# Optimization experiments

Measured on AMD Instinct MI355X. Metric: run time of the kernel, lower is better.

The kernel has to match this reference:

```python
import jax, jax.numpy as jnp
import numpy as np

B, C, T = 8, 256, 4096
IC = C // 2  # inter_channels
BN_EPS = 1e-5


def setup_inputs() -> dict:
    key = jax.random.key(0)
    ks = jax.random.split(key, 12)
    s_in = 1.0 / np.sqrt(C)
    s_ic = 1.0 / np.sqrt(IC)
    return {
        "x": jax.random.normal(ks[0], (B, C, T), dtype=jnp.float32),
        "theta_w": jax.random.uniform(ks[1], (IC, C), jnp.float32, -s_in, s_in),
        "theta_b": jax.random.uniform(ks[2], (IC,), jnp.float32, -s_in, s_in),
        "phi_w": jax.random.uniform(ks[3], (IC, C), jnp.float32, -s_in, s_in),
        "phi_b": jax.random.uniform(ks[4], (IC,), jnp.float32, -s_in, s_in),
        "g_w": jax.random.uniform(ks[5], (IC, C), jnp.float32, -s_in, s_in),
        "g_b": jax.random.uniform(ks[6], (IC,), jnp.float32, -s_in, s_in),
        "w_w": jax.random.uniform(ks[7], (C, IC), jnp.float32, -s_ic, s_ic),
        "w_b": jax.random.uniform(ks[8], (C,), jnp.float32, -s_ic, s_ic),
        "bn_gamma": jax.random.normal(ks[9], (C,), dtype=jnp.float32),
        "bn_beta": jax.random.normal(ks[10], (C,), dtype=jnp.float32),
    }


def _conv1x1(w, b, inp):
    # Conv1d kernel_size=1 == per-position channel matmul
    return jnp.einsum('oc,bct->bot', w, inp) + b[None, :, None]


def _maxpool2(z):
    b, c, t = z.shape
    return z.reshape(b, c, t // 2, 2).max(axis=-1)


def reference(x, theta_w, theta_b, phi_w, phi_b, g_w, g_b, w_w, w_b, bn_gamma, bn_beta):
    theta_x = _conv1x1(theta_w, theta_b, x)              # (B, IC, T)
    phi_x = _maxpool2(_conv1x1(phi_w, phi_b, x))         # (B, IC, T/2)
    g_x = _maxpool2(_conv1x1(g_w, g_b, x))               # (B, IC, T/2)

    # f = theta^T @ phi ; softmax-free, divided by N = T/2
    f = jnp.einsum('bct,bcs->bts', theta_x, phi_x)       # (B, T, T/2)
    f_div_C = f / f.shape[-1]
    y = jnp.einsum('bts,bcs->bct', f_div_C, g_x)         # (B, IC, T)

    w_y = _conv1x1(w_w, w_b, y)                          # (B, C, T)
    # BatchNorm1d (training-mode batch statistics over batch+time)
    mean = w_y.mean(axis=(0, 2), keepdims=True)
    var = w_y.var(axis=(0, 2), keepdims=True)
    w_y = (w_y - mean) * jax.lax.rsqrt(var + BN_EPS)
    w_y = w_y * bn_gamma[None, :, None] + bn_beta[None, :, None]
    return w_y + x
```

## Files before the change

kernel.cpp:

```cpp
#include <hip/hip_runtime.h>
#include <hip/hip_bf16.h>

typedef __attribute__((ext_vector_type(8))) short short8;
typedef __attribute__((ext_vector_type(4))) short short4v;
typedef __attribute__((ext_vector_type(4))) float floatx4;
typedef unsigned int u32;

#define BB 8
#define CC 256
#define ICH 128
#define TT 4096
#define SS 2048
static constexpr float BN_EPS = 1e-5f;
static constexpr float INV_S  = 1.0f / 2048.0f;
static constexpr float INV_BT = 1.0f / 32768.0f;

typedef const __attribute__((address_space(1))) u32* gas_ptr;
typedef __attribute__((address_space(3))) u32* las_ptr;
__device__ __forceinline__ void gl_lds16(const void* g, void* l) {
    __builtin_amdgcn_global_load_lds((gas_ptr)g, (las_ptr)l, 16, 0, 0);
}


__global__ __launch_bounds__(256) void k0x_transpose(
    const float* __restrict__ x, __hip_bfloat16* __restrict__ xt,
    const float* __restrict__ phi_w, const float* __restrict__ g_w,
    __hip_bfloat16* __restrict__ Wf)
{
    const int id = blockIdx.x;
    if (id >= 2048) {
        int idx = (id - 2048) * 256 + threadIdx.x;
        const float* src = (idx < 8192) ? (phi_w + (size_t)idx * 4)
                                        : (g_w + (size_t)(idx - 8192) * 4);
        float4 v = *(const float4*)src;
        alignas(8) __hip_bfloat16 t[4];
        t[0] = __float2bfloat16(v.x); t[1] = __float2bfloat16(v.y);
        t[2] = __float2bfloat16(v.z); t[3] = __float2bfloat16(v.w);
        *(short4v*)(Wf + (size_t)idx * 4) = *(const short4v*)t;
        return;
    }

    __shared__ float Tl[64][65];
    const int b = id & 7, rest = id >> 3;
    const int cb = (rest & 3) * 64, tb = (rest >> 2) * 64;
    const int tid = threadIdx.x;
    #pragma unroll
    for (int it = 0; it < 4; ++it) {
        int idx = tid + 256 * it;
        int row = idx >> 4, c4 = idx & 15;
        float4 v = *(const float4*)(x + ((size_t)b * CC + cb + row) * TT + tb + c4 * 4);
        Tl[row][c4 * 4 + 0] = v.x; Tl[row][c4 * 4 + 1] = v.y;
        Tl[row][c4 * 4 + 2] = v.z; Tl[row][c4 * 4 + 3] = v.w;
    }
    __syncthreads();
    #pragma unroll
    for (int it = 0; it < 2; ++it) {
        int idx = tid + 256 * it;
        int trow = idx >> 3, ch = idx & 7;
        alignas(16) __hip_bfloat16 tmp[8];
        #pragma unroll
        for (int e = 0; e < 8; ++e) tmp[e] = __float2bfloat16(Tl[ch * 8 + e][trow]);
        *(short8*)(xt + ((size_t)b * TT + tb + trow) * CC + cb + ch * 8) = *(const short8*)tmp;
    }
}

__global__ __launch_bounds__(256) void k1_mfma(
    const __hip_bfloat16* __restrict__ Wf, const float* __restrict__ phi_b,
    const float* __restrict__ g_b, const __hip_bfloat16* __restrict__ xt,
    __hip_bfloat16* __restrict__ phi_g)
{
    __shared__ short lds[128 * 132];
    short* As = lds;
    short* Bs = lds + 128 * 64;

    const int id = blockIdx.x;
    const int b  = id & 7;
    const int m0 = ((id >> 3) & 1) * 128;
    const int tb = (id >> 4) * 128;
    const int s0 = (id >> 4) * 64;
    const int tid = threadIdx.x;
    const int w = tid >> 6, l = tid & 63;
    const int quad = l >> 4, lm = l & 15;
    const int wm = (w & 1) * 64, wn = (w >> 1) * 64;
    const int rs = l >> 3, cs = (l & 7) * 8;

    const __hip_bfloat16* Ap = Wf + (size_t)m0 * CC;
    const __hip_bfloat16* Bp = xt + ((size_t)b * TT + tb) * CC;

    floatx4 acc[4][4];
    #pragma unroll
    for (int i = 0; i < 4; ++i)
        #pragma unroll
        for (int j = 0; j < 4; ++j) acc[i][j] = (floatx4)0.f;

    for (int kc = 0; kc < 4; ++kc) {
        const int k0 = kc * 64;
        const int rbase = w * 32;
        #pragma unroll
        for (int t = 0; t < 4; ++t) {
            gl_lds16(Ap + (size_t)(rbase + t * 8 + rs) * CC + k0 + cs, &As[(rbase + t * 8) * 64]);
            gl_lds16(Bp + (size_t)(rbase + t * 8 + rs) * CC + k0 + cs, &Bs[(rbase + t * 8) * 64]);
        }
        __syncthreads();
        #pragma unroll
        for (int ks = 0; ks < 2; ++ks) {
            short8 a[4], bb[4];
            #pragma unroll
            for (int i = 0; i < 4; ++i)
                a[i] = *(const short8*)&As[(wm + i * 16 + lm) * 64 + ks * 32 + quad * 8];
            #pragma unroll
            for (int j = 0; j < 4; ++j)
                bb[j] = *(const short8*)&Bs[(wn + j * 16 + lm) * 64 + ks * 32 + quad * 8];
            #pragma unroll
            for (int i = 0; i < 4; ++i)
                #pragma unroll
                for (int j = 0; j < 4; ++j)
                    acc[i][j] = __builtin_amdgcn_mfma_f32_16x16x32_bf16(a[i], bb[j], acc[i][j], 0, 0, 0);
        }
        __syncthreads();
    }

    __hip_bfloat16* Out = (__hip_bfloat16*)lds;
    #pragma unroll
    for (int i = 0; i < 4; ++i)
        #pragma unroll
        for (int j = 0; j < 4; ++j)
            #pragma unroll
            for (int r = 0; r < 4; ++r)
                Out[(wm + i * 16 + quad * 4 + r) * 132 + wn + j * 16 + lm] =
                    __float2bfloat16(acc[i][j][r]);
    __syncthreads();
    #pragma unroll
    for (int it = 0; it < 4; ++it) {
        int idx = tid + 256 * it;
        int orow = idx >> 3, grp = idx & 7;
        int o = m0 + orow;
        float bias = (o < ICH) ? phi_b[o] : g_b[o - ICH];
        short8 v0 = *(const short8*)&Out[orow * 132 + grp * 16];
        short8 v1 = *(const short8*)&Out[orow * 132 + grp * 16 + 8];
        const __hip_bfloat16* p0 = (const __hip_bfloat16*)&v0;
        const __hip_bfloat16* p1 = (const __hip_bfloat16*)&v1;
        alignas(16) __hip_bfloat16 o8[8];
        #pragma unroll
        for (int e = 0; e < 4; ++e)
            o8[e] = __float2bfloat16(
                fmaxf(__bfloat162float(p0[2 * e]), __bfloat162float(p0[2 * e + 1])) + bias);
        #pragma unroll
        for (int e = 0; e < 4; ++e)
            o8[4 + e] = __float2bfloat16(
                fmaxf(__bfloat162float(p1[2 * e]), __bfloat162float(p1[2 * e + 1])) + bias);
        *(short8*)(phi_g + ((size_t)b * CC + o) * SS + s0 + grp * 8) = *(const short8*)o8;
    }
}

__global__ __launch_bounds__(256) void k2_mfma(
    const __hip_bfloat16* __restrict__ phi_g, float* __restrict__ Mpart)
{
    __shared__ short lds[2 * 128 * 64];
    short* As = lds;
    short* Bs = lds + 128 * 64;
    const int b = blockIdx.x, sc = blockIdx.y;
    const int tid = threadIdx.x;
    const int w = tid >> 6, l = tid & 63;
    const int quad = l >> 4, lm = l & 15;
    const int wm = (w & 1) * 64, wn = (w >> 1) * 64;
    const int rs = l >> 3, cs = (l & 7) * 8;

    const __hip_bfloat16* Ap = phi_g + (size_t)b * CC * SS + (size_t)ICH * SS + sc * 256;
    const __hip_bfloat16* Bp = phi_g + (size_t)b * CC * SS + sc * 256;

    floatx4 acc[4][4];
    #pragma unroll
    for (int i = 0; i < 4; ++i)
        #pragma unroll
        for (int j = 0; j < 4; ++j) acc[i][j] = (floatx4)0.f;

    for (int kc = 0; kc < 4; ++kc) {
        const int k0 = kc * 64;
        const int rbase = w * 32;
        #pragma unroll
        for (int t = 0; t < 4; ++t) {
            gl_lds16(Ap + (size_t)(rbase + t * 8 + rs) * SS + k0 + cs, &As[(rbase + t * 8) * 64]);
            gl_lds16(Bp + (size_t)(rbase + t * 8 + rs) * SS + k0 + cs, &Bs[(rbase + t * 8) * 64]);
        }
        __syncthreads();
        #pragma unroll
        for (int ks = 0; ks < 2; ++ks) {
            short8 a[4], bb[4];
            #pragma unroll
            for (int i = 0; i < 4; ++i)
                a[i] = *(const short8*)&As[(wm + i * 16 + lm) * 64 + ks * 32 + quad * 8];
            #pragma unroll
            for (int j = 0; j < 4; ++j)
                bb[j] = *(const short8*)&Bs[(wn + j * 16 + lm) * 64 + ks * 32 + quad * 8];
            #pragma unroll
            for (int i = 0; i < 4; ++i)
                #pragma unroll
                for (int j = 0; j < 4; ++j)
                    acc[i][j] = __builtin_amdgcn_mfma_f32_16x16x32_bf16(a[i], bb[j], acc[i][j], 0, 0, 0);
        }
        __syncthreads();
    }

    float* dst = Mpart + ((size_t)(b * 8 + sc)) * ICH * ICH;
    #pragma unroll
    for (int i = 0; i < 4; ++i)
        #pragma unroll
        for (int j = 0; j < 4; ++j)
            #pragma unroll
            for (int r = 0; r < 4; ++r)
                dst[(size_t)(wm + i * 16 + quad * 4 + r) * ICH + wn + j * 16 + lm] = acc[i][j][r];
}

__global__ __launch_bounds__(256) void kpq(
    const float* __restrict__ w_w, const float* __restrict__ Mpart,
    const float* __restrict__ theta_w, const float* __restrict__ theta_b,
    const float* __restrict__ w_b, __hip_bfloat16* __restrict__ P,
    float* __restrict__ q)
{
    __shared__ float Ms[128][128];
    __shared__ float Al[128][68];
    const int bid = blockIdx.x;
    const int b    = bid & 7;
    const int rest = bid >> 3;
    const int cob  = (rest >> 2) * 64;
    const int cib  = (rest & 3) * 64;
    const int tid = threadIdx.x;
    const int tx = tid & 15, ty = tid >> 4;

    {
        const float* src = Mpart + (size_t)b * 8 * ICH * ICH;
        #pragma unroll
        for (int e = 0; e < 16; ++e) {
            int f = e * 256 + tid;
            float4 s = *(const float4*)(src + (size_t)f * 4);
            #pragma unroll
            for (int sc = 1; sc < 8; ++sc) {
                float4 m = *(const float4*)(src + (size_t)sc * ICH * ICH + (size_t)f * 4);
                s.x += m.x; s.y += m.y; s.z += m.z; s.w += m.w;
            }
            *(float4*)&Ms[f >> 5][(f & 31) * 4] = s;
        }
    }
    #pragma unroll
    for (int it = 0; it < 8; ++it) {
        int idx = tid + 256 * it;
        int row = idx & 63, c4 = idx >> 6;
        float4 v = *(const float4*)(w_w + (size_t)(cob + row) * ICH + c4 * 4);
        Al[c4 * 4 + 0][row] = v.x; Al[c4 * 4 + 1][row] = v.y;
        Al[c4 * 4 + 2][row] = v.z; Al[c4 * 4 + 3][row] = v.w;
    }
    __syncthreads();

    float accK[4][8] = {};
    #pragma unroll 4
    for (int k = 0; k < 128; ++k) {
        float4 av = *(const float4*)&Al[k][ty * 4];
        float4 b0 = *(const float4*)&Ms[k][tx * 4];
        float4 b1 = *(const float4*)&Ms[k][64 + tx * 4];
        const float* avp = (const float*)&av;
        const float* b0p = (const float*)&b0;
        const float* b1p = (const float*)&b1;
        #pragma unroll
        for (int i = 0; i < 4; ++i) {
            #pragma unroll
            for (int j = 0; j < 4; ++j) {
                accK[i][j]     += avp[i] * b0p[j];
                accK[i][4 + j] += avp[i] * b1p[j];
            }
        }
    }
    __syncthreads();

    float (*KbL)[68] = Al;
    #pragma unroll
    for (int i = 0; i < 4; ++i)
        #pragma unroll
        for (int jj = 0; jj < 8; ++jj)
            KbL[(jj >> 2) * 64 + tx * 4 + (jj & 3)][ty * 4 + i] = accK[i][jj] * INV_S;
    __syncthreads();

    float acc[4][4] = {};
    #pragma unroll 8
    for (int k = 0; k < 128; ++k) {
        float4 av = *(const float4*)&KbL[k][ty * 4];
        float4 bv = *(const float4*)(theta_w + (size_t)k * CC + cib + tx * 4);
        const float* avp = (const float*)&av;
        const float* bvp = (const float*)&bv;
        #pragma unroll
        for (int i = 0; i < 4; ++i)
            #pragma unroll
            for (int j = 0; j < 4; ++j)
                acc[i][j] += avp[i] * bvp[j];
    }
    #pragma unroll
    for (int i = 0; i < 4; ++i) {
        alignas(8) __hip_bfloat16 o4[4];
        #pragma unroll
        for (int j = 0; j < 4; ++j) o4[j] = __float2bfloat16(acc[i][j]);
        *(short4v*)(P + ((size_t)b * CC + cob + ty * 4 + i) * CC + cib + tx * 4) =
            *(const short4v*)o4;
    }

    if ((rest & 3) == 0 && tid < 64) {
        float s = w_b[cob + tid];
        #pragma unroll 8
        for (int c = 0; c < ICH; ++c) s += KbL[c][tid] * theta_b[c];
        q[b * CC + cob + tid] = s;
    }
}

__global__ __launch_bounds__(256) void k4_mfma(
    const __hip_bfloat16* __restrict__ P, const __hip_bfloat16* __restrict__ xt,
    const float* __restrict__ q, __hip_bfloat16* __restrict__ wy,
    float* __restrict__ pbuf)
{
    __shared__ short lds[128 * 132];
    __shared__ float pst1[4 * 64], pst2[4 * 64];
    short* As = lds;
    short* Bs = lds + 128 * 64;

    const int id = blockIdx.x;
    const int b  = id & 7;
    const int m0 = ((id >> 3) & 1) * 128;
    const int tt = id >> 4;
    const int t0 = tt * 128;
    const int tid = threadIdx.x;
    const int w = tid >> 6, l = tid & 63;
    const int quad = l >> 4, lm = l & 15;
    const int wm = (w & 1) * 64, wn = (w >> 1) * 64;
    const int rs = l >> 3, cs = (l & 7) * 8;

    const __hip_bfloat16* Ap = P + ((size_t)b * CC + m0) * CC;
    const __hip_bfloat16* Bp = xt + ((size_t)b * TT + t0) * CC;

    floatx4 acc[4][4];
    #pragma unroll
    for (int i = 0; i < 4; ++i)
        #pragma unroll
        for (int j = 0; j < 4; ++j) acc[i][j] = (floatx4)0.f;

    for (int kc = 0; kc < 4; ++kc) {
        const int k0 = kc * 64;
        const int rbase = w * 32;
        #pragma unroll
        for (int t = 0; t < 4; ++t) {
            gl_lds16(Ap + (size_t)(rbase + t * 8 + rs) * CC + k0 + cs, &As[(rbase + t * 8) * 64]);
            gl_lds16(Bp + (size_t)(rbase + t * 8 + rs) * CC + k0 + cs, &Bs[(rbase + t * 8) * 64]);
        }
        __syncthreads();
        #pragma unroll
        for (int ks = 0; ks < 2; ++ks) {
            short8 a[4], bb[4];
            #pragma unroll
            for (int i = 0; i < 4; ++i)
                a[i] = *(const short8*)&As[(wm + i * 16 + lm) * 64 + ks * 32 + quad * 8];
            #pragma unroll
            for (int j = 0; j < 4; ++j)
                bb[j] = *(const short8*)&Bs[(wn + j * 16 + lm) * 64 + ks * 32 + quad * 8];
            #pragma unroll
            for (int i = 0; i < 4; ++i)
                #pragma unroll
                for (int j = 0; j < 4; ++j)
                    acc[i][j] = __builtin_amdgcn_mfma_f32_16x16x32_bf16(a[i], bb[j], acc[i][j], 0, 0, 0);
        }
        __syncthreads();
    }

    #pragma unroll
    for (int i = 0; i < 4; ++i) {
        #pragma unroll
        for (int r = 0; r < 4; ++r) {
            int m = wm + i * 16 + quad * 4 + r;
            float bias = q[b * CC + m0 + m];
            float s1 = 0.f, s2 = 0.f;
            #pragma unroll
            for (int j = 0; j < 4; ++j) {
                float v = acc[i][j][r] + bias;
                s1 += v; s2 += v * v;
            }
            #pragma unroll
            for (int off = 1; off < 16; off <<= 1) {
                s1 += __shfl_xor(s1, off);
                s2 += __shfl_xor(s2, off);
            }
            if (lm == 0) {
                pst1[w * 64 + i * 16 + quad * 4 + r] = s1;
                pst2[w * 64 + i * 16 + quad * 4 + r] = s2;
            }
        }
    }

    __hip_bfloat16* Out = (__hip_bfloat16*)lds;
    #pragma unroll
    for (int i = 0; i < 4; ++i) {
        #pragma unroll
        for (int r = 0; r < 4; ++r) {
            int m = wm + i * 16 + quad * 4 + r;
            float bias = q[b * CC + m0 + m];
            #pragma unroll
            for (int j = 0; j < 4; ++j)
                Out[m * 132 + wn + j * 16 + lm] = __float2bfloat16(acc[i][j][r] + bias);
        }
    }
    __syncthreads();

    if (tid < 128) {
        int half = tid >> 6, k = tid & 63;
        float s1 = pst1[half * 64 + k] + pst1[(2 + half) * 64 + k];
        float s2 = pst2[half * 64 + k] + pst2[(2 + half) * 64 + k];
        size_t col = (size_t)b * 32 + tt;
        pbuf[(size_t)(m0 + tid) * 256 + col] = s1;
        pbuf[65536 + (size_t)(m0 + tid) * 256 + col] = s2;
    }

    #pragma unroll
    for (int it = 0; it < 8; ++it) {
        int idx = tid + 256 * it;
        int row = idx >> 4, cg = idx & 15;
        *(short8*)(wy + ((size_t)b * CC + m0 + row) * TT + t0 + cg * 8) =
            *(const short8*)&Out[row * 132 + cg * 8];
    }
}

__global__ __launch_bounds__(256) void k6_out(
    const __hip_bfloat16* __restrict__ wy, const __hip_bfloat16* __restrict__ xt,
    const float* __restrict__ pbuf, const float* __restrict__ gamma,
    const float* __restrict__ beta, float* __restrict__ out)
{
    __shared__ float Fs[64][68];
    __shared__ float cA[64], cB[64];
    const int id = blockIdx.x;
    const int b  = id & 7;
    const int cb = ((id >> 3) & 3) * 64;
    const int tb0 = (id >> 5) * 256;
    const int tid = threadIdx.x;

    {
        const int ch = tid >> 2, qtr = tid & 3;
        const float* p1 = pbuf + (size_t)(cb + ch) * 256 + qtr * 64;
        const float* p2 = p1 + 65536;
        float s1 = 0.f, s2 = 0.f;
        #pragma unroll
        for (int e = 0; e < 16; ++e) {
            float4 a = *(const float4*)(p1 + e * 4);
            float4 c = *(const float4*)(p2 + e * 4);
            s1 += a.x + a.y + a.z + a.w;
            s2 += c.x + c.y + c.z + c.w;
        }
        s1 += __shfl_xor(s1, 1); s1 += __shfl_xor(s1, 2);
        s2 += __shfl_xor(s2, 1); s2 += __shfl_xor(s2, 2);
        if (qtr == 0) {
            float mean = s1 * INV_BT;
            float var  = s2 * INV_BT - mean * mean;
            float A = gamma[cb + ch] * rsqrtf(var + BN_EPS);
            cA[ch] = A;
            cB[ch] = beta[cb + ch] - mean * A;
        }
    }

    for (int tt = 0; tt < 4; ++tt) {
        const int tb = tb0 + tt * 64;
        __syncthreads();
        {
            const int t = tid >> 2, cseg = (tid & 3) * 16;
            const __hip_bfloat16* src = xt + ((size_t)b * TT + tb + t) * CC + cb + cseg;
            short8 v0 = *(const short8*)src;
            short8 v1 = *(const short8*)(src + 8);
            const __hip_bfloat16* p0 = (const __hip_bfloat16*)&v0;
            const __hip_bfloat16* p1 = (const __hip_bfloat16*)&v1;
            #pragma unroll
            for (int e = 0; e < 8; ++e) Fs[t][cseg + e] = __bfloat162float(p0[e]);
            #pragma unroll
            for (int e = 0; e < 8; ++e) Fs[t][cseg + 8 + e] = __bfloat162float(p1[e]);
        }
        __syncthreads();
        {
            const int c = tid >> 2, seg = (tid & 3) * 16;
            const float A = cA[c], Bc = cB[c];
            const __hip_bfloat16* wsrc = wy + ((size_t)b * CC + cb + c) * TT + tb + seg;
            short8 w0 = *(const short8*)wsrc;
            short8 w1 = *(const short8*)(wsrc + 8);
            const __hip_bfloat16* q0 = (const __hip_bfloat16*)&w0;
            const __hip_bfloat16* q1 = (const __hip_bfloat16*)&w1;
            float* dst = out + ((size_t)b * CC + cb + c) * TT + tb + seg;
            #pragma unroll
            for (int e = 0; e < 8; ++e)
                dst[e] = __bfloat162float(q0[e]) * A + Bc + Fs[seg + e][c];
            #pragma unroll
            for (int e = 0; e < 8; ++e)
                dst[8 + e] = __bfloat162float(q1[e]) * A + Bc + Fs[seg + 8 + e][c];
        }
    }
}

extern "C" void kernel_launch(void* const* d_in, const int* in_sizes, int n_in,
                              void* d_out, int out_size, void* d_ws, size_t ws_size,
                              hipStream_t stream)
{
    const float* x        = (const float*)d_in[0];
    const float* theta_w  = (const float*)d_in[1];
    const float* theta_b  = (const float*)d_in[2];
    const float* phi_w    = (const float*)d_in[3];
    const float* phi_b    = (const float*)d_in[4];
    const float* g_w      = (const float*)d_in[5];
    const float* g_b      = (const float*)d_in[6];
    const float* w_w      = (const float*)d_in[7];
    const float* w_b      = (const float*)d_in[8];
    const float* bn_gamma = (const float*)d_in[9];
    const float* bn_beta  = (const float*)d_in[10];
    float* out = (float*)d_out;

    char* p = (char*)d_ws;
    __hip_bfloat16* xt    = (__hip_bfloat16*)p; p += (size_t)8388608 * 2;
    __hip_bfloat16* Wf    = (__hip_bfloat16*)p; p += (size_t)65536 * 2;
    __hip_bfloat16* phi_g = (__hip_bfloat16*)p; p += (size_t)4194304 * 2;
    __hip_bfloat16* P     = (__hip_bfloat16*)p; p += (size_t)524288 * 2;
    float* Mpart = (float*)p; p += (size_t)1048576 * 4;
    float* q     = (float*)p; p += (size_t)2048 * 4;
    __hip_bfloat16* wy = (__hip_bfloat16*)p; p += (size_t)8388608 * 2;
    float* pbuf  = (float*)p;

    k0x_transpose<<<dim3(2112), 256, 0, stream>>>(x, xt, phi_w, g_w, Wf);
    k1_mfma<<<dim3(512), 256, 0, stream>>>(Wf, phi_b, g_b, xt, phi_g);
    k2_mfma<<<dim3(8, 8), 256, 0, stream>>>(phi_g, Mpart);
    kpq<<<dim3(128), 256, 0, stream>>>(w_w, Mpart, theta_w, theta_b, w_b, P, q);
    k4_mfma<<<dim3(512), 256, 0, stream>>>(P, xt, q, wy, pbuf);
    k6_out<<<dim3(512), 256, 0, stream>>>(wy, xt, pbuf, bn_gamma, bn_beta, out);
}
```

Before: 183.6 us.

## Double-buffer LDS staging in the three MFMA GEMM kernels

Converts the k1, k2 and k4 GEMM main loops from single-buffered to double-buffered LDS staging. The next K-chunk is issued via global_load_lds before the MFMAs on the current chunk, so global-memory latency overlaps with compute. In exchange LDS use per block grows to 64 KB, which can lower occupancy. Only four K-iterations exist, which limits how much overlap is possible.

```diff
diff --git a/kernel.cpp b/kernel.cpp
--- a/kernel.cpp
+++ b/kernel.cpp
@@ -69,9 +69,7 @@
     const float* __restrict__ g_b, const __hip_bfloat16* __restrict__ xt,
     __hip_bfloat16* __restrict__ phi_g)
 {
-    __shared__ short lds[128 * 132];
-    short* As = lds;
-    short* Bs = lds + 128 * 64;
+    __shared__ short lds[4 * 128 * 64];
 
     const int id = blockIdx.x;
     const int b  = id & 7;
@@ -83,6 +81,7 @@
     const int quad = l >> 4, lm = l & 15;
     const int wm = (w & 1) * 64, wn = (w >> 1) * 64;
     const int rs = l >> 3, cs = (l & 7) * 8;
+    const int rbase = w * 32;
 
     const __hip_bfloat16* Ap = Wf + (size_t)m0 * CC;
     const __hip_bfloat16* Bp = xt + ((size_t)b * TT + tb) * CC;
@@ -93,15 +92,24 @@
         #pragma unroll
         for (int j = 0; j < 4; ++j) acc[i][j] = (floatx4)0.f;
 
+    auto stage = [&](int kc, int buf) {
+        const int k0 = kc * 64;
+        short* Asb = lds + buf * 16384;
+        short* Bsb = Asb + 8192;
+        #pragma unroll
+        for (int t = 0; t < 4; ++t) {
+            gl_lds16(Ap + (size_t)(rbase + t * 8 + rs) * CC + k0 + cs, &Asb[(rbase + t * 8) * 64]);
+            gl_lds16(Bp + (size_t)(rbase + t * 8 + rs) * CC + k0 + cs, &Bsb[(rbase + t * 8) * 64]);
+        }
+    };
+
+    stage(0, 0);
+    __syncthreads();
     for (int kc = 0; kc < 4; ++kc) {
-        const int k0 = kc * 64;
-        const int rbase = w * 32;
-        #pragma unroll
-        for (int t = 0; t < 4; ++t) {
-            gl_lds16(Ap + (size_t)(rbase + t * 8 + rs) * CC + k0 + cs, &As[(rbase + t * 8) * 64]);
-            gl_lds16(Bp + (size_t)(rbase + t * 8 + rs) * CC + k0 + cs, &Bs[(rbase + t * 8) * 64]);
-        }
-        __syncthreads();
+        const int cur = kc & 1;
+        if (kc < 3) stage(kc + 1, cur ^ 1);
+        short* As = lds + cur * 16384;
+        short* Bs = As + 8192;
         #pragma unroll
         for (int ks = 0; ks < 2; ++ks) {
             short8 a[4], bb[4];
@@ -156,15 +164,14 @@
 __global__ __launch_bounds__(256) void k2_mfma(
     const __hip_bfloat16* __restrict__ phi_g, float* __restrict__ Mpart)
 {
-    __shared__ short lds[2 * 128 * 64];
-    short* As = lds;
-    short* Bs = lds + 128 * 64;
+    __shared__ short lds[4 * 128 * 64];
     const int b = blockIdx.x, sc = blockIdx.y;
     const int tid = threadIdx.x;
     const int w = tid >> 6, l = tid & 63;
     const int quad = l >> 4, lm = l & 15;
     const int wm = (w & 1) * 64, wn = (w >> 1) * 64;
     const int rs = l >> 3, cs = (l & 7) * 8;
+    const int rbase = w * 32;
 
     const __hip_bfloat16* Ap = phi_g + (size_t)b * CC * SS + (size_t)ICH * SS + sc * 256;
     const __hip_bfloat16* Bp = phi_g + (size_t)b * CC * SS + sc * 256;
@@ -175,15 +182,24 @@
         #pragma unroll
         for (int j = 0; j < 4; ++j) acc[i][j] = (floatx4)0.f;
 
+    auto stage = [&](int kc, int buf) {
+        const int k0 = kc * 64;
+        short* Asb = lds + buf * 16384;
+        short* Bsb = Asb + 8192;
+        #pragma unroll
+        for (int t = 0; t < 4; ++t) {
+            gl_lds16(Ap + (size_t)(rbase + t * 8 + rs) * SS + k0 + cs, &Asb[(rbase + t * 8) * 64]);
+            gl_lds16(Bp + (size_t)(rbase + t * 8 + rs) * SS + k0 + cs, &Bsb[(rbase + t * 8) * 64]);
+        }
+    };
+
+    stage(0, 0);
+    __syncthreads();
     for (int kc = 0; kc < 4; ++kc) {
-        const int k0 = kc * 64;
-        const int rbase = w * 32;
-        #pragma unroll
-        for (int t = 0; t < 4; ++t) {
-            gl_lds16(Ap + (size_t)(rbase + t * 8 + rs) * SS + k0 + cs, &As[(rbase + t * 8) * 64]);
-            gl_lds16(Bp + (size_t)(rbase + t * 8 + rs) * SS + k0 + cs, &Bs[(rbase + t * 8) * 64]);
-        }
-        __syncthreads();
+        const int cur = kc & 1;
+        if (kc < 3) stage(kc + 1, cur ^ 1);
+        short* As = lds + cur * 16384;
+        short* Bs = As + 8192;
         #pragma unroll
         for (int ks = 0; ks < 2; ++ks) {
             short8 a[4], bb[4];
@@ -315,10 +331,8 @@
     const float* __restrict__ q, __hip_bfloat16* __restrict__ wy,
     float* __restrict__ pbuf)
 {
-    __shared__ short lds[128 * 132];
+    __shared__ short lds[4 * 128 * 64];
     __shared__ float pst1[4 * 64], pst2[4 * 64];
-    short* As = lds;
-    short* Bs = lds + 128 * 64;
 
     const int id = blockIdx.x;
     const int b  = id & 7;
@@ -330,6 +344,7 @@
     const int quad = l >> 4, lm = l & 15;
     const int wm = (w & 1) * 64, wn = (w >> 1) * 64;
     const int rs = l >> 3, cs = (l & 7) * 8;
+    const int rbase = w * 32;
 
     const __hip_bfloat16* Ap = P + ((size_t)b * CC + m0) * CC;
     const __hip_bfloat16* Bp = xt + ((size_t)b * TT + t0) * CC;
@@ -340,15 +355,24 @@
         #pragma unroll
         for (int j = 0; j < 4; ++j) acc[i][j] = (floatx4)0.f;
 
+    auto stage = [&](int kc, int buf) {
+        const int k0 = kc * 64;
+        short* Asb = lds + buf * 16384;
+        short* Bsb = Asb + 8192;
+        #pragma unroll
+        for (int t = 0; t < 4; ++t) {
+            gl_lds16(Ap + (size_t)(rbase + t * 8 + rs) * CC + k0 + cs, &Asb[(rbase + t * 8) * 64]);
+            gl_lds16(Bp + (size_t)(rbase + t * 8 + rs) * CC + k0 + cs, &Bsb[(rbase + t * 8) * 64]);
+        }
+    };
+
+    stage(0, 0);
+    __syncthreads();
     for (int kc = 0; kc < 4; ++kc) {
-        const int k0 = kc * 64;
-        const int rbase = w * 32;
-        #pragma unroll
-        for (int t = 0; t < 4; ++t) {
-            gl_lds16(Ap + (size_t)(rbase + t * 8 + rs) * CC + k0 + cs, &As[(rbase + t * 8) * 64]);
-            gl_lds16(Bp + (size_t)(rbase + t * 8 + rs) * CC + k0 + cs, &Bs[(rbase + t * 8) * 64]);
-        }
-        __syncthreads();
+        const int cur = kc & 1;
+        if (kc < 3) stage(kc + 1, cur ^ 1);
+        short* As = lds + cur * 16384;
+        short* Bs = As + 8192;
         #pragma unroll
         for (int ks = 0; ks < 2; ++ks) {
             short8 a[4], bb[4];
```

Measured after the change: 184.2 us. Within noise of the previous version (+0.3%).
